# Performance work log

Measured on AMD Instinct MI355X. Metric: run time of the kernel, lower is better.

The kernel has to match this reference:

```python
import jax, jax.numpy as jnp
import numpy as np

NUM_HEADS = 16
ROPE_THETA = 10000.0


def setup_inputs() -> dict:
    key = jax.random.key(0)
    k1, k2, k3 = jax.random.split(key, 3)
    B, T, C = 2, 2048, 1024
    x = jax.random.normal(k1, (B, T, C), dtype=jnp.float32)
    w_qkv = jax.random.normal(k2, (3 * C, C), dtype=jnp.float32) * 0.02
    w_out = jax.random.normal(k3, (C, C), dtype=jnp.float32) * 0.02
    return {"x": x, "w_qkv": w_qkv, "w_out": w_out}


def _apply_rope(x, cos, sin):
    # x: (B, H, T, D); interleaved complex pairs: (x[...,2i], x[...,2i+1])
    B, H, T, D = x.shape
    xp = x.reshape(B, H, T, D // 2, 2)
    xr, xi = xp[..., 0], xp[..., 1]
    # cos/sin: (T, D//2) broadcast over (B, H)
    out_r = xr * cos - xi * sin
    out_i = xr * sin + xi * cos
    return jnp.stack([out_r, out_i], axis=-1).reshape(B, H, T, D)


def reference(x, w_qkv, w_out):
    B, T, C = x.shape
    H = NUM_HEADS
    D = C // H
    scale = 1.0 / np.sqrt(D).astype(np.float32)

    qkv = x @ w_qkv.T                      # (B, T, 3C)
    q, k, v = jnp.split(qkv, 3, axis=-1)

    def to_heads(t):
        return t.reshape(B, T, H, D).transpose(0, 2, 1, 3)  # (B, H, T, D)

    q, k, v = to_heads(q), to_heads(k), to_heads(v)

    # RoPE frequencies: freqs[t, j] = t / theta^(2j/D)
    inv_freq = 1.0 / (ROPE_THETA ** (jnp.arange(0, D, 2, dtype=jnp.float32) / D))
    freqs = jnp.arange(T, dtype=jnp.float32)[:, None] * inv_freq[None, :]  # (T, D//2)
    cos, sin = jnp.cos(freqs), jnp.sin(freqs)

    q = _apply_rope(q, cos, sin)
    k = _apply_rope(k, cos, sin)

    att = jnp.einsum('bhqd,bhkd->bhqk', q, k) * scale   # (B, H, T, T)
    causal = jnp.tril(jnp.ones((T, T), dtype=bool))
    att = jnp.where(causal[None, None], att, -jnp.inf)
    att = jax.nn.softmax(att, axis=-1)
    # dropout p=0.0 (eval) -> identity

    out = jnp.einsum('bhqk,bhkd->bhqd', att, v)          # (B, H, T, D)
    out = out.transpose(0, 2, 1, 3).reshape(B, T, C)
    return out @ w_out.T
```

## Files before the change

### kernel.cpp

```cpp
#include <hip/hip_runtime.h>
#include <hip/hip_bf16.h>
#include <math.h>

#define DEV __device__ __forceinline__

typedef float  floatx4 __attribute__((ext_vector_type(4)));
typedef short  bf16x8  __attribute__((ext_vector_type(8)));

typedef __attribute__((address_space(1))) void gvoid;
typedef __attribute__((address_space(3))) void lvoid;

static constexpr int Bc = 2, Tc = 2048, Cc = 1024, Hc = 16, Dc = 64;

DEV void gload16(const void* g, void* l) {
    __builtin_amdgcn_global_load_lds((gvoid*)g, (lvoid*)l, 16, 0, 0);
}

__global__ void prep_kernel(const float* __restrict__ xf,
                            const float* __restrict__ wqkvf,
                            const float* __restrict__ woutf,
                            __hip_bfloat16* __restrict__ xb,
                            __hip_bfloat16* __restrict__ wqkvb,
                            __hip_bfloat16* __restrict__ woutb,
                            float* __restrict__ cosT, float* __restrict__ sinT) {
    int gb = blockIdx.x;
    if (gb < 8192) {
        const float* src; __hip_bfloat16* dst; int i;
        if (gb < 4096)      { src = xf;    dst = xb;    i = gb * 256 + threadIdx.x; }
        else if (gb < 7168) { src = wqkvf; dst = wqkvb; i = (gb - 4096) * 256 + threadIdx.x; }
        else                { src = woutf; dst = woutb; i = (gb - 7168) * 256 + threadIdx.x; }
        float4 f = ((const float4*)src)[i];
        union { ushort4 u; __hip_bfloat16 h[4]; } pk;
        pk.h[0] = __float2bfloat16(f.x);
        pk.h[1] = __float2bfloat16(f.y);
        pk.h[2] = __float2bfloat16(f.z);
        pk.h[3] = __float2bfloat16(f.w);
        ((ushort4*)dst)[i] = pk.u;
    } else {
        int i = (gb - 8192) * 256 + threadIdx.x;
        int t = i >> 5, j = i & 31;
        float invf = powf(10000.0f, -(float)j / 32.0f);
        float f = (float)t * invf;
        cosT[i] = cosf(f);
        sinT[i] = sinf(f);
    }
}

template <int EPI>
__global__ __launch_bounds__(256, 2) void gemm_bt(
    const __hip_bfloat16* __restrict__ A,
    const __hip_bfloat16* __restrict__ Bm,
    float* __restrict__ Cout,
    __hip_bfloat16* __restrict__ qb,
    __hip_bfloat16* __restrict__ kb,
    __hip_bfloat16* __restrict__ vb,
    const float* __restrict__ cosT,
    const float* __restrict__ sinT,
    int K)
{
    __shared__ __align__(16) __hip_bfloat16 As[128 * 64];
    __shared__ __align__(16) __hip_bfloat16 Bs[128 * 64];

    const int tid  = threadIdx.x;
    const int lane = tid & 63, wave = tid >> 6;
    const int quad = lane >> 4, cidx = lane & 15;
    const int wm = wave & 1, wn = wave >> 1;
    const int bm = blockIdx.x * 128, bn = blockIdx.y * 128;

    floatx4 acc[4][4] = {};

    for (int k0 = 0; k0 < K; k0 += 64) {
#pragma unroll
        for (int it = 0; it < 4; ++it) {
            int idx = tid + it * 256;
            int r = idx >> 3, cs = idx & 7;
            int cg = cs ^ (r & 7);
            gload16(A  + (size_t)(bm + r) * K + k0 + cg * 8, As + idx * 8);
            gload16(Bm + (size_t)(bn + r) * K + k0 + cg * 8, Bs + idx * 8);
        }
        __syncthreads();
#pragma unroll
        for (int ks = 0; ks < 2; ++ks) {
            bf16x8 af[4], bf[4];
#pragma unroll
            for (int mt = 0; mt < 4; ++mt) {
                int r = wm * 64 + mt * 16 + cidx;
                af[mt] = *(const bf16x8*)(As + (r * 8 + ((ks * 4 + quad) ^ (r & 7))) * 8);
            }
#pragma unroll
            for (int nt = 0; nt < 4; ++nt) {
                int r = wn * 64 + nt * 16 + cidx;
                bf[nt] = *(const bf16x8*)(Bs + (r * 8 + ((ks * 4 + quad) ^ (r & 7))) * 8);
            }
#pragma unroll
            for (int mt = 0; mt < 4; ++mt)
#pragma unroll
                for (int nt = 0; nt < 4; ++nt)
                    acc[mt][nt] = __builtin_amdgcn_mfma_f32_16x16x32_bf16(
                        af[mt], bf[nt], acc[mt][nt], 0, 0, 0);
        }
        __syncthreads();
    }

    if constexpr (EPI == 0) {
#pragma unroll
        for (int mt = 0; mt < 4; ++mt)
#pragma unroll
            for (int nt = 0; nt < 4; ++nt) {
                int n = bn + wn * 64 + nt * 16 + cidx;
#pragma unroll
                for (int reg = 0; reg < 4; ++reg) {
                    int m = bm + wm * 64 + mt * 16 + quad * 4 + reg;
                    Cout[(size_t)m * 1024 + n] = acc[mt][nt][reg];
                }
            }
    } else {
        const float SL2E = 0.125f * 1.44269504088896f;
#pragma unroll
        for (int nt = 0; nt < 4; ++nt) {
            int n   = bn + wn * 64 + nt * 16 + cidx;
            int sec = n >> 10;
            int cc  = n & 1023;
            int h = cc >> 6, d = cc & 63, j = d >> 1;
#pragma unroll
            for (int mt = 0; mt < 4; ++mt) {
#pragma unroll
                for (int reg = 0; reg < 4; ++reg) {
                    int m = bm + wm * 64 + mt * 16 + quad * 4 + reg;
                    int b = m >> 11, t = m & 2047;
                    float v = acc[mt][nt][reg];
                    float p = __shfl_xor(v, 1);
                    if (sec == 2) {
                        vb[((size_t)(b * Hc + h) * Dc + d) * Tc + t] = __float2bfloat16(v);
                    } else {
                        float cz = cosT[t * 32 + j];
                        float sz = sinT[t * 32 + j];
                        float o = (d & 1) ? (p * sz + v * cz) : (v * cz - p * sz);
                        if (sec == 0) o *= SL2E;
                        __hip_bfloat16* dst = (sec == 0) ? qb : kb;
                        dst[((size_t)(b * Hc + h) * Tc + t) * Dc + d] = __float2bfloat16(o);
                    }
                }
            }
        }
    }
}

__global__ __launch_bounds__(256, 2) void attn_kernel(
    const __hip_bfloat16* __restrict__ qb,
    const __hip_bfloat16* __restrict__ kb,
    const __hip_bfloat16* __restrict__ vb,
    __hip_bfloat16* __restrict__ ob)
{
    __shared__ __align__(16) __hip_bfloat16 Qs[64 * 64];
    __shared__ __align__(16) __hip_bfloat16 Ks[128 * 64];
    __shared__ __align__(16) __hip_bfloat16 Vt[64 * 128];
    __shared__ __align__(16) __hip_bfloat16 Ps[4][16 * 128];

    const int tid  = threadIdx.x;
    const int lane = tid & 63, wave = tid >> 6;
    const int quad = lane >> 4, cidx = lane & 15;
    const int bh = blockIdx.y;
    const int b = bh >> 4, h = bh & 15;
    const size_t plane = (size_t)bh * Tc * Dc;
    const __hip_bfloat16* Vp = vb + plane;

    for (int half = 0; half < 2; ++half) {
        const int qt = half ? (int)blockIdx.x : 31 - (int)blockIdx.x;
        const int qbase = qt * 64;

#pragma unroll
        for (int it = 0; it < 2; ++it) {
            int idx = tid + it * 256;
            int r = idx >> 3, cs = idx & 7;
            int cg = cs ^ (r & 7);
            gload16(qb + plane + (size_t)(qbase + r) * 64 + cg * 8, Qs + idx * 8);
        }
        __syncthreads();

        bf16x8 qf[2];
#pragma unroll
        for (int ks = 0; ks < 2; ++ks) {
            int r = wave * 16 + cidx;
            qf[ks] = *(const bf16x8*)(Qs + (r * 8 + ((ks * 4 + quad) ^ (r & 7))) * 8);
        }

        floatx4 oacc[4] = {};
        float lsum[4] = {0.f, 0.f, 0.f, 0.f};
        const int ktmax = (qbase + 63) >> 7;

        for (int kt = 0; kt <= ktmax; ++kt) {
#pragma unroll
            for (int it = 0; it < 4; ++it) {
                int idx = tid + it * 256;
                int r = idx >> 3, cs = idx & 7;
                int cg = cs ^ (r & 7);
                gload16(kb + plane + (size_t)(kt * 128 + r) * 64 + cg * 8, Ks + idx * 8);
            }
#pragma unroll
            for (int it = 0; it < 4; ++it) {
                int idx = tid + it * 256;
                int r = idx >> 4, cs = idx & 15;
                int c = cs ^ (r & 15);
                gload16(Vp + (size_t)r * Tc + kt * 128 + c * 8, Vt + idx * 8);
            }
            __syncthreads();

            floatx4 sacc[8] = {};
#pragma unroll
            for (int ks = 0; ks < 2; ++ks) {
#pragma unroll
                for (int nt = 0; nt < 8; ++nt) {
                    int r = nt * 16 + cidx;
                    bf16x8 kf = *(const bf16x8*)(Ks + (r * 8 + ((ks * 4 + quad) ^ (r & 7))) * 8);
                    sacc[nt] = __builtin_amdgcn_mfma_f32_16x16x32_bf16(qf[ks], kf, sacc[nt], 0, 0, 0);
                }
            }

            const bool domask = (kt == ktmax);
#pragma unroll
            for (int nt = 0; nt < 8; ++nt) {
                int n = kt * 128 + nt * 16 + cidx;
#pragma unroll
                for (int reg = 0; reg < 4; ++reg) {
                    int m = qbase + wave * 16 + quad * 4 + reg;
                    float p = exp2f(sacc[nt][reg]);
                    if (domask && n > m) p = 0.0f;
                    sacc[nt][reg] = p;
                    lsum[reg] += p;
                }
            }

            __hip_bfloat16* myP = &Ps[wave][0];
#pragma unroll
            for (int nt = 0; nt < 8; ++nt)
#pragma unroll
                for (int reg = 0; reg < 4; ++reg) {
                    int r = quad * 4 + reg;
                    int col = nt * 16 + cidx;
                    myP[(r * 16 + ((col >> 3) ^ r)) * 8 + (col & 7)] =
                        __float2bfloat16(sacc[nt][reg]);
                }
#pragma unroll
            for (int ks = 0; ks < 4; ++ks) {
                bf16x8 af = *(const bf16x8*)(myP + (cidx * 16 + ((ks * 4 + quad) ^ cidx)) * 8);
#pragma unroll
                for (int dt = 0; dt < 4; ++dt) {
                    int dr = dt * 16 + cidx;
                    bf16x8 vf = *(const bf16x8*)(Vt + (dr * 16 + ((ks * 4 + quad) ^ (dr & 15))) * 8);
                    oacc[dt] = __builtin_amdgcn_mfma_f32_16x16x32_bf16(af, vf, oacc[dt], 0, 0, 0);
                }
            }
            __syncthreads();
        }

#pragma unroll
        for (int off = 1; off < 16; off <<= 1)
#pragma unroll
            for (int reg = 0; reg < 4; ++reg)
                lsum[reg] += __shfl_xor(lsum[reg], off);

#pragma unroll
        for (int dt = 0; dt < 4; ++dt)
#pragma unroll
            for (int reg = 0; reg < 4; ++reg) {
                int t = qbase + wave * 16 + quad * 4 + reg;
                float v = oacc[dt][reg] / lsum[reg];
                ob[(size_t)(b * Tc + t) * Cc + h * 64 + dt * 16 + cidx] = __float2bfloat16(v);
            }
    }
}

extern "C" void kernel_launch(void* const* d_in, const int* in_sizes, int n_in,
                              void* d_out, int out_size, void* d_ws, size_t ws_size,
                              hipStream_t stream) {
    const float* xf = nullptr; const float* wqkvf = nullptr; const float* woutf = nullptr;
    for (int i = 0; i < n_in; ++i) {
        if      (in_sizes[i] == 2 * 2048 * 1024) xf    = (const float*)d_in[i];
        else if (in_sizes[i] == 3 * 1024 * 1024) wqkvf = (const float*)d_in[i];
        else if (in_sizes[i] == 1024 * 1024)     woutf = (const float*)d_in[i];
    }
    float* out = (float*)d_out;

    char* ws = (char*)d_ws;
    const size_t MB = 1024 * 1024;
    __hip_bfloat16* qb    = (__hip_bfloat16*)(ws);
    __hip_bfloat16* kb    = (__hip_bfloat16*)(ws + 8  * MB);
    __hip_bfloat16* vb    = (__hip_bfloat16*)(ws + 16 * MB);
    __hip_bfloat16* ab    = (__hip_bfloat16*)(ws + 24 * MB);
    float* cosT           = (float*)(ws + 32 * MB);
    float* sinT           = (float*)(ws + 32 * MB + 256 * 1024);
    __hip_bfloat16* xb    = (__hip_bfloat16*)(ws + 33 * MB);
    __hip_bfloat16* wqkvb = (__hip_bfloat16*)(ws + 41 * MB);
    __hip_bfloat16* woutb = (__hip_bfloat16*)(ws + 47 * MB);

    prep_kernel<<<dim3(8448), dim3(256), 0, stream>>>(
        xf, wqkvf, woutf, xb, wqkvb, woutb, cosT, sinT);

    gemm_bt<1><<<dim3(32, 24), dim3(256), 0, stream>>>(
        xb, wqkvb, nullptr, qb, kb, vb, cosT, sinT, 1024);
    attn_kernel<<<dim3(16, 32), dim3(256), 0, stream>>>(qb, kb, vb, ab);
    gemm_bt<0><<<dim3(32, 8), dim3(256), 0, stream>>>(
        ab, woutb, out, nullptr, nullptr, nullptr, nullptr, nullptr, 1024);
}
```

Baseline: 196.5 us.

## Stage V-transpose epilogue through LDS and give each attention query tile its own block

The QKV GEMM epilogue now writes V tiles into shared memory and stores them transposed to the V^T layout with coalesced 16-byte writes, replacing scattered 2-byte strided stores. The attention kernel drops the paired-tile loop: each block handles one query tile, so the grid doubles and heavy tiles are ordered first. The Q staging buffer reuses Ks to cut LDS, launch bounds allow three blocks per CU, and exp2f becomes the hardware builtin. Load balance now relies on the scheduler rather than explicit pairing, and the higher occupancy target may constrain registers.

```diff
diff --git a/kernel.cpp b/kernel.cpp
--- a/kernel.cpp
+++ b/kernel.cpp
@@ -58,8 +58,9 @@
     const float* __restrict__ sinT,
     int K)
 {
-    __shared__ __align__(16) __hip_bfloat16 As[128 * 64];
-    __shared__ __align__(16) __hip_bfloat16 Bs[128 * 64];
+    __shared__ __align__(16) __hip_bfloat16 SM[2 * 128 * 64];
+    __hip_bfloat16* const As = SM;
+    __hip_bfloat16* const Bs = SM + 128 * 64;
 
     const int tid  = threadIdx.x;
     const int lane = tid & 63, wave = tid >> 6;
@@ -114,6 +115,33 @@
                     Cout[(size_t)m * 1024 + n] = acc[mt][nt][reg];
                 }
             }
+    } else if (bn >= 2048) {
+#pragma unroll
+        for (int nt = 0; nt < 4; ++nt) {
+            int n_l = wn * 64 + nt * 16 + cidx;
+#pragma unroll
+            for (int mt = 0; mt < 4; ++mt)
+#pragma unroll
+                for (int reg = 0; reg < 4; ++reg) {
+                    int m_l = wm * 64 + mt * 16 + quad * 4 + reg;
+                    SM[n_l * 128 + (((m_l >> 3) ^ (n_l & 15)) * 8) + (m_l & 7)] =
+                        __float2bfloat16(acc[mt][nt][reg]);
+                }
+        }
+        __syncthreads();
+        {
+            int row = tid >> 1, hf = tid & 1;
+            int cc = (bn - 2048) + row;
+            int h = cc >> 6, d = cc & 63;
+            int b = bm >> 11, t0 = bm & 2047;
+            __hip_bfloat16* dstrow = vb + ((size_t)(b * Hc + h) * Dc + d) * Tc + t0;
+#pragma unroll
+            for (int i = 0; i < 8; ++i) {
+                int c = hf * 8 + i;
+                *(uint4*)(dstrow + c * 8) =
+                    *(const uint4*)(SM + row * 128 + ((c ^ (row & 15)) * 8));
+            }
+        }
     } else {
         const float SL2E = 0.125f * 1.44269504088896f;
 #pragma unroll
@@ -122,6 +150,7 @@
             int sec = n >> 10;
             int cc  = n & 1023;
             int h = cc >> 6, d = cc & 63, j = d >> 1;
+            __hip_bfloat16* dst = (sec == 0) ? qb : kb;
 #pragma unroll
             for (int mt = 0; mt < 4; ++mt) {
 #pragma unroll
@@ -130,29 +159,23 @@
                     int b = m >> 11, t = m & 2047;
                     float v = acc[mt][nt][reg];
                     float p = __shfl_xor(v, 1);
-                    if (sec == 2) {
-                        vb[((size_t)(b * Hc + h) * Dc + d) * Tc + t] = __float2bfloat16(v);
-                    } else {
-                        float cz = cosT[t * 32 + j];
-                        float sz = sinT[t * 32 + j];
-                        float o = (d & 1) ? (p * sz + v * cz) : (v * cz - p * sz);
-                        if (sec == 0) o *= SL2E;
-                        __hip_bfloat16* dst = (sec == 0) ? qb : kb;
-                        dst[((size_t)(b * Hc + h) * Tc + t) * Dc + d] = __float2bfloat16(o);
-                    }
+                    float cz = cosT[t * 32 + j];
+                    float sz = sinT[t * 32 + j];
+                    float o = (d & 1) ? (p * sz + v * cz) : (v * cz - p * sz);
+                    if (sec == 0) o *= SL2E;
+                    dst[((size_t)(b * Hc + h) * Tc + t) * Dc + d] = __float2bfloat16(o);
                 }
             }
         }
     }
 }
 
-__global__ __launch_bounds__(256, 2) void attn_kernel(
+__global__ __launch_bounds__(256, 3) void attn_kernel(
     const __hip_bfloat16* __restrict__ qb,
     const __hip_bfloat16* __restrict__ kb,
     const __hip_bfloat16* __restrict__ vb,
     __hip_bfloat16* __restrict__ ob)
 {
-    __shared__ __align__(16) __hip_bfloat16 Qs[64 * 64];
     __shared__ __align__(16) __hip_bfloat16 Ks[128 * 64];
     __shared__ __align__(16) __hip_bfloat16 Vt[64 * 128];
     __shared__ __align__(16) __hip_bfloat16 Ps[4][16 * 128];
@@ -165,110 +188,109 @@
     const size_t plane = (size_t)bh * Tc * Dc;
     const __hip_bfloat16* Vp = vb + plane;
 
-    for (int half = 0; half < 2; ++half) {
-        const int qt = half ? (int)blockIdx.x : 31 - (int)blockIdx.x;
-        const int qbase = qt * 64;
-
-#pragma unroll
-        for (int it = 0; it < 2; ++it) {
+    const int qt = 31 - (int)blockIdx.x;
+    const int qbase = qt * 64;
+
+#pragma unroll
+    for (int it = 0; it < 2; ++it) {
+        int idx = tid + it * 256;
+        int r = idx >> 3, cs = idx & 7;
+        int cg = cs ^ (r & 7);
+        gload16(qb + plane + (size_t)(qbase + r) * 64 + cg * 8, Ks + idx * 8);
+    }
+    __syncthreads();
+
+    bf16x8 qf[2];
+#pragma unroll
+    for (int ks = 0; ks < 2; ++ks) {
+        int r = wave * 16 + cidx;
+        qf[ks] = *(const bf16x8*)(Ks + (r * 8 + ((ks * 4 + quad) ^ (r & 7))) * 8);
+    }
+    __syncthreads();
+
+    floatx4 oacc[4] = {};
+    float lsum[4] = {0.f, 0.f, 0.f, 0.f};
+    const int ktmax = (qbase + 63) >> 7;
+
+    for (int kt = 0; kt <= ktmax; ++kt) {
+#pragma unroll
+        for (int it = 0; it < 4; ++it) {
             int idx = tid + it * 256;
             int r = idx >> 3, cs = idx & 7;
             int cg = cs ^ (r & 7);
-            gload16(qb + plane + (size_t)(qbase + r) * 64 + cg * 8, Qs + idx * 8);
-        }
-        __syncthreads();
-
-        bf16x8 qf[2];
+            gload16(kb + plane + (size_t)(kt * 128 + r) * 64 + cg * 8, Ks + idx * 8);
+        }
+#pragma unroll
+        for (int it = 0; it < 4; ++it) {
+            int idx = tid + it * 256;
+            int r = idx >> 4, cs = idx & 15;
+            int c = cs ^ (r & 15);
+            gload16(Vp + (size_t)r * Tc + kt * 128 + c * 8, Vt + idx * 8);
+        }
+        __syncthreads();
+
+        floatx4 sacc[8] = {};
 #pragma unroll
         for (int ks = 0; ks < 2; ++ks) {
-            int r = wave * 16 + cidx;
-            qf[ks] = *(const bf16x8*)(Qs + (r * 8 + ((ks * 4 + quad) ^ (r & 7))) * 8);
-        }
-
-        floatx4 oacc[4] = {};
-        float lsum[4] = {0.f, 0.f, 0.f, 0.f};
-        const int ktmax = (qbase + 63) >> 7;
-
-        for (int kt = 0; kt <= ktmax; ++kt) {
-#pragma unroll
-            for (int it = 0; it < 4; ++it) {
-                int idx = tid + it * 256;
-                int r = idx >> 3, cs = idx & 7;
-                int cg = cs ^ (r & 7);
-                gload16(kb + plane + (size_t)(kt * 128 + r) * 64 + cg * 8, Ks + idx * 8);
-            }
-#pragma unroll
-            for (int it = 0; it < 4; ++it) {
-                int idx = tid + it * 256;
-                int r = idx >> 4, cs = idx & 15;
-                int c = cs ^ (r & 15);
-                gload16(Vp + (size_t)r * Tc + kt * 128 + c * 8, Vt + idx * 8);
-            }
-            __syncthreads();
-
-            floatx4 sacc[8] = {};
-#pragma unroll
-            for (int ks = 0; ks < 2; ++ks) {
-#pragma unroll
-                for (int nt = 0; nt < 8; ++nt) {
-                    int r = nt * 16 + cidx;
-                    bf16x8 kf = *(const bf16x8*)(Ks + (r * 8 + ((ks * 4 + quad) ^ (r & 7))) * 8);
-                    sacc[nt] = __builtin_amdgcn_mfma_f32_16x16x32_bf16(qf[ks], kf, sacc[nt], 0, 0, 0);
-                }
-            }
-
-            const bool domask = (kt == ktmax);
 #pragma unroll
             for (int nt = 0; nt < 8; ++nt) {
-                int n = kt * 128 + nt * 16 + cidx;
-#pragma unroll
-                for (int reg = 0; reg < 4; ++reg) {
-                    int m = qbase + wave * 16 + quad * 4 + reg;
-                    float p = exp2f(sacc[nt][reg]);
-                    if (domask && n > m) p = 0.0f;
-                    sacc[nt][reg] = p;
-                    lsum[reg] += p;
-                }
-            }
-
-            __hip_bfloat16* myP = &Ps[wave][0];
-#pragma unroll
-            for (int nt = 0; nt < 8; ++nt)
-#pragma unroll
-                for (int reg = 0; reg < 4; ++reg) {
-                    int r = quad * 4 + reg;
-                    int col = nt * 16 + cidx;
-                    myP[(r * 16 + ((col >> 3) ^ r)) * 8 + (col & 7)] =
-                        __float2bfloat16(sacc[nt][reg]);
-                }
-#pragma unroll
-            for (int ks = 0; ks < 4; ++ks) {
-                bf16x8 af = *(const bf16x8*)(myP + (cidx * 16 + ((ks * 4 + quad) ^ cidx)) * 8);
-#pragma unroll
-                for (int dt = 0; dt < 4; ++dt) {
-                    int dr = dt * 16 + cidx;
-                    bf16x8 vf = *(const bf16x8*)(Vt + (dr * 16 + ((ks * 4 + quad) ^ (dr & 15))) * 8);
-                    oacc[dt] = __builtin_amdgcn_mfma_f32_16x16x32_bf16(af, vf, oacc[dt], 0, 0, 0);
-                }
-            }
-            __syncthreads();
-        }
-
-#pragma unroll
-        for (int off = 1; off < 16; off <<= 1)
-#pragma unroll
-            for (int reg = 0; reg < 4; ++reg)
-                lsum[reg] += __shfl_xor(lsum[reg], off);
-
-#pragma unroll
-        for (int dt = 0; dt < 4; ++dt)
+                int r = nt * 16 + cidx;
+                bf16x8 kf = *(const bf16x8*)(Ks + (r * 8 + ((ks * 4 + quad) ^ (r & 7))) * 8);
+                sacc[nt] = __builtin_amdgcn_mfma_f32_16x16x32_bf16(qf[ks], kf, sacc[nt], 0, 0, 0);
+            }
+        }
+
+        const bool domask = (kt == ktmax);
+#pragma unroll
+        for (int nt = 0; nt < 8; ++nt) {
+            int n = kt * 128 + nt * 16 + cidx;
 #pragma unroll
             for (int reg = 0; reg < 4; ++reg) {
-                int t = qbase + wave * 16 + quad * 4 + reg;
-                float v = oacc[dt][reg] / lsum[reg];
-                ob[(size_t)(b * Tc + t) * Cc + h * 64 + dt * 16 + cidx] = __float2bfloat16(v);
-            }
-    }
+                int m = qbase + wave * 16 + quad * 4 + reg;
+                float p = __builtin_amdgcn_exp2f(sacc[nt][reg]);
+                if (domask && n > m) p = 0.0f;
+                sacc[nt][reg] = p;
+                lsum[reg] += p;
+            }
+        }
+
+        __hip_bfloat16* myP = &Ps[wave][0];
+#pragma unroll
+        for (int nt = 0; nt < 8; ++nt)
+#pragma unroll
+            for (int reg = 0; reg < 4; ++reg) {
+                int r = quad * 4 + reg;
+                int col = nt * 16 + cidx;
+                myP[(r * 16 + ((col >> 3) ^ r)) * 8 + (col & 7)] =
+                    __float2bfloat16(sacc[nt][reg]);
+            }
+#pragma unroll
+        for (int ks = 0; ks < 4; ++ks) {
+            bf16x8 af = *(const bf16x8*)(myP + (cidx * 16 + ((ks * 4 + quad) ^ cidx)) * 8);
+#pragma unroll
+            for (int dt = 0; dt < 4; ++dt) {
+                int dr = dt * 16 + cidx;
+                bf16x8 vf = *(const bf16x8*)(Vt + (dr * 16 + ((ks * 4 + quad) ^ (dr & 15))) * 8);
+                oacc[dt] = __builtin_amdgcn_mfma_f32_16x16x32_bf16(af, vf, oacc[dt], 0, 0, 0);
+            }
+        }
+        __syncthreads();
+    }
+
+#pragma unroll
+    for (int off = 1; off < 16; off <<= 1)
+#pragma unroll
+        for (int reg = 0; reg < 4; ++reg)
+            lsum[reg] += __shfl_xor(lsum[reg], off);
+
+#pragma unroll
+    for (int dt = 0; dt < 4; ++dt)
+#pragma unroll
+        for (int reg = 0; reg < 4; ++reg) {
+            int t = qbase + wave * 16 + quad * 4 + reg;
+            float v = oacc[dt][reg] / lsum[reg];
+            ob[(size_t)(b * Tc + t) * Cc + h * 64 + dt * 16 + cidx] = __float2bfloat16(v);
+        }
 }
 
 extern "C" void kernel_launch(void* const* d_in, const int* in_sizes, int n_in,
@@ -299,7 +321,7 @@
 
     gemm_bt<1><<<dim3(32, 24), dim3(256), 0, stream>>>(
         xb, wqkvb, nullptr, qb, kb, vb, cosT, sinT, 1024);
-    attn_kernel<<<dim3(16, 32), dim3(256), 0, stream>>>(qb, kb, vb, ab);
+    attn_kernel<<<dim3(32, 32), dim3(256), 0, stream>>>(qb, kb, vb, ab);
     gemm_bt<0><<<dim3(32, 8), dim3(256), 0, stream>>>(
         ab, woutb, out, nullptr, nullptr, nullptr, nullptr, nullptr, 1024);
 }
```

Result: slower. 213.2 us (+8.5%).
